# Performance work log

Measured on AMD Instinct MI355X. Metric: run time of the kernel, lower is better.

Reference implementation:

```python
import jax, jax.numpy as jnp
import numpy as np

TOP_K = 2  # module uses global top_k=2

def setup_inputs() -> dict:
    key = jax.random.key(0)
    k1, k2, k3 = jax.random.split(key, 3)
    B, S, D, E = 4, 4096, 2048, 64
    x = jax.random.normal(k1, (B, S, D), dtype=jnp.float32)
    W = jax.random.normal(k2, (E, D), dtype=jnp.float32) * 0.02  # gate_linear weight (no bias)
    noise_weight = jnp.zeros((E,), dtype=jnp.float32)  # nn.Parameter(torch.zeros(E))
    noise = jax.random.normal(k3, (B, S, E), dtype=jnp.float32)  # randn_like(logits) * noisy_std(=1.0)
    return {"x": x, "W": W, "noise_weight": noise_weight, "noise": noise}

def reference(x, W, noise_weight, noise):
    # logits = gate_linear(x)
    logits = jnp.einsum('bsd,ed->bse', x, W)
    # noisy logits: noise * noise_weight (per-expert scale), added to logits
    logits_noisy = logits + noise * noise_weight
    # top-k (largest, sorted descending, like torch.topk)
    top_vals, top_idx = jax.lax.top_k(logits_noisy, TOP_K)  # [B,S,k]
    B, S, E = logits_noisy.shape
    # scatter top-k values into -inf tensor along expert dim
    sparse = jnp.full_like(logits_noisy, -jnp.inf)
    b_ix = jnp.arange(B)[:, None, None]
    s_ix = jnp.arange(S)[None, :, None]
    sparse = sparse.at[b_ix, s_ix, top_idx].set(top_vals)
    # softmax over experts; exp(-inf)=0 zeros out non-selected experts
    gated_probs = jax.nn.softmax(sparse, axis=-1)
    return (gated_probs, top_idx, top_vals)
```

## Files before the change

kernel.cpp:

```cpp
#include <hip/hip_runtime.h>
#include <math.h>


typedef __attribute__((ext_vector_type(8))) __bf16 bf16x8;
typedef __attribute__((ext_vector_type(8))) unsigned short u16x8;
typedef __attribute__((ext_vector_type(4))) float f32x4;

constexpr int EXPN = 64;
constexpr int BM   = 32;
constexpr int BK   = 64;
constexpr int LDK  = BK + 8;

__device__ __forceinline__ void split2(float f, unsigned short& h, unsigned short& l) {
    const unsigned b = __float_as_uint(f);
    h = (unsigned short)(b >> 16);
    const float fh = __uint_as_float(b & 0xffff0000u);
    l = (unsigned short)(__float_as_uint(f - fh) >> 16);
}

__global__ __launch_bounds__(256)
void moe_gate_kernel(const float* __restrict__ x,
                     const float* __restrict__ W,
                     const float* __restrict__ nw,
                     const float* __restrict__ noise,
                     float* __restrict__ probs,
                     float* __restrict__ idx_out,
                     float* __restrict__ val_out,
                     int D)
{
    __shared__ unsigned short xh[2][BM][LDK], xl[2][BM][LDK];
    __shared__ unsigned short wh[2][EXPN][LDK], wl[2][EXPN][LDK];
    __shared__ float ls[BM][EXPN + 1];

    const int tid  = threadIdx.x;
    const int lane = tid & 63;
    const int wv   = tid >> 6;
    const int hh   = wv & 1;
    const int qq   = wv >> 1;
    const int m0   = blockIdx.x * BM;

    const int xrow = tid >> 3;
    const int xcol = (tid & 7) * 8;
    const int wrow = tid >> 2;
    const int wcol = (tid & 3) * 16;

    const float* xbase = x + (size_t)(m0 + xrow) * D + xcol;
    const float* wbase = W + (size_t)wrow * D + wcol;

    f32x4 acc0 = {0.f, 0.f, 0.f, 0.f};
    f32x4 acc1 = {0.f, 0.f, 0.f, 0.f};

    float4 xr0, xr1, wr0, wr1, wr2, wr3;
    xr0 = *(const float4*)(xbase);
    xr1 = *(const float4*)(xbase + 4);
    wr0 = *(const float4*)(wbase);
    wr1 = *(const float4*)(wbase + 4);
    wr2 = *(const float4*)(wbase + 8);
    wr3 = *(const float4*)(wbase + 12);

    const int nchunk = D / BK;
    const int fr = lane & 15;
    const int kq = (lane >> 4) * 8;

    for (int c = 0; c < nchunk; ++c) {
        const int buf = c & 1;

        {
            const float xv[8] = {xr0.x, xr0.y, xr0.z, xr0.w,
                                 xr1.x, xr1.y, xr1.z, xr1.w};
            u16x8 hv, lv;
#pragma unroll
            for (int i = 0; i < 8; ++i) {
                unsigned short a, b; split2(xv[i], a, b);
                hv[i] = a; lv[i] = b;
            }
            *(u16x8*)&xh[buf][xrow][xcol] = hv;
            *(u16x8*)&xl[buf][xrow][xcol] = lv;

            const float wvv[16] = {wr0.x, wr0.y, wr0.z, wr0.w,
                                   wr1.x, wr1.y, wr1.z, wr1.w,
                                   wr2.x, wr2.y, wr2.z, wr2.w,
                                   wr3.x, wr3.y, wr3.z, wr3.w};
            u16x8 h0, l0, h1, l1;
#pragma unroll
            for (int i = 0; i < 8; ++i) {
                unsigned short a, b; split2(wvv[i], a, b);
                h0[i] = a; l0[i] = b;
                split2(wvv[i + 8], a, b);
                h1[i] = a; l1[i] = b;
            }
            *(u16x8*)&wh[buf][wrow][wcol]     = h0;
            *(u16x8*)&wl[buf][wrow][wcol]     = l0;
            *(u16x8*)&wh[buf][wrow][wcol + 8] = h1;
            *(u16x8*)&wl[buf][wrow][wcol + 8] = l1;
        }
        __syncthreads();

        if (c + 1 < nchunk) {
            const float* xp = xbase + (c + 1) * BK;
            xr0 = *(const float4*)(xp);
            xr1 = *(const float4*)(xp + 4);
            const float* wp = wbase + (c + 1) * BK;
            wr0 = *(const float4*)(wp);
            wr1 = *(const float4*)(wp + 4);
            wr2 = *(const float4*)(wp + 8);
            wr3 = *(const float4*)(wp + 12);
        }

#pragma unroll
        for (int ks = 0; ks < BK; ks += 32) {
            const bf16x8 ah  = *(const bf16x8*)&xh[buf][hh * 16 + fr][ks + kq];
            const bf16x8 al  = *(const bf16x8*)&xl[buf][hh * 16 + fr][ks + kq];
            const bf16x8 b0h = *(const bf16x8*)&wh[buf][qq * 32 + fr][ks + kq];
            const bf16x8 b0l = *(const bf16x8*)&wl[buf][qq * 32 + fr][ks + kq];
            const bf16x8 b1h = *(const bf16x8*)&wh[buf][qq * 32 + 16 + fr][ks + kq];
            const bf16x8 b1l = *(const bf16x8*)&wl[buf][qq * 32 + 16 + fr][ks + kq];
            acc0 = __builtin_amdgcn_mfma_f32_16x16x32_bf16(ah, b0h, acc0, 0, 0, 0);
            acc0 = __builtin_amdgcn_mfma_f32_16x16x32_bf16(ah, b0l, acc0, 0, 0, 0);
            acc0 = __builtin_amdgcn_mfma_f32_16x16x32_bf16(al, b0h, acc0, 0, 0, 0);
            acc1 = __builtin_amdgcn_mfma_f32_16x16x32_bf16(ah, b1h, acc1, 0, 0, 0);
            acc1 = __builtin_amdgcn_mfma_f32_16x16x32_bf16(ah, b1l, acc1, 0, 0, 0);
            acc1 = __builtin_amdgcn_mfma_f32_16x16x32_bf16(al, b1h, acc1, 0, 0, 0);
        }
    }

    const int trow = hh * 16 + (lane >> 4) * 4;
#pragma unroll
    for (int r = 0; r < 4; ++r) {
        ls[trow + r][qq * 32 + fr]      = acc0[r];
        ls[trow + r][qq * 32 + 16 + fr] = acc1[r];
    }
    __syncthreads();

    const float nwv = nw[lane];

#pragma unroll 1
    for (int t = 0; t < 8; ++t) {
        const int tl = wv * 8 + t;
        const int g  = m0 + tl;
        const float logit = fmaf(noise[(size_t)g * EXPN + lane], nwv, ls[tl][lane]);

        float v0; int i0;
        {
            float v = logit; int ix = lane;
#pragma unroll
            for (int off = 32; off; off >>= 1) {
                const float vo = __shfl_xor(v, off);
                const int   io = __shfl_xor(ix, off);
                if (vo > v || (vo == v && io < ix)) { v = vo; ix = io; }
            }
            v0 = v; i0 = ix;
        }
        float v1; int i1;
        {
            float v = (lane == i0) ? -INFINITY : logit; int ix = lane;
#pragma unroll
            for (int off = 32; off; off >>= 1) {
                const float vo = __shfl_xor(v, off);
                const int   io = __shfl_xor(ix, off);
                if (vo > v || (vo == v && io < ix)) { v = vo; ix = io; }
            }
            v1 = v; i1 = ix;
        }
        float v2; int i2;
        {
            float v = (lane == i0 || lane == i1) ? -INFINITY : logit; int ix = lane;
#pragma unroll
            for (int off = 32; off; off >>= 1) {
                const float vo = __shfl_xor(v, off);
                const int   io = __shfl_xor(ix, off);
                if (vo > v || (vo == v && io < ix)) { v = vo; ix = io; }
            }
            v2 = v; i2 = ix;
        }

        const float eps = 1e-3f;
        if ((v0 - v1) < eps || (v1 - v2) < eps) {
            const float* xr  = x + (size_t)g * D;
            const float* w0r = W + (size_t)i0 * D;
            const float* w1r = W + (size_t)i1 * D;
            const float* w2r = W + (size_t)i2 * D;
            double s0 = 0.0, s1 = 0.0, s2 = 0.0;
            for (int d = lane; d < D; d += 64) {
                const double xv = (double)xr[d];
                s0 += xv * (double)w0r[d];
                s1 += xv * (double)w1r[d];
                s2 += xv * (double)w2r[d];
            }
#pragma unroll
            for (int off = 32; off; off >>= 1) {
                s0 += __shfl_xor(s0, off);
                s1 += __shfl_xor(s1, off);
                s2 += __shfl_xor(s2, off);
            }
            double d0 = s0 + (double)noise[(size_t)g * EXPN + i0] * (double)nw[i0];
            double d1 = s1 + (double)noise[(size_t)g * EXPN + i1] * (double)nw[i1];
            double d2 = s2 + (double)noise[(size_t)g * EXPN + i2] * (double)nw[i2];
            #define CSWAP(va, ia, vb, ib)                                   \
                if ((vb > va) || (vb == va && ib < ia)) {                   \
                    double tv = va; va = vb; vb = tv;                       \
                    int ti = ia; ia = ib; ib = ti; }
            CSWAP(d0, i0, d1, i1)
            CSWAP(d1, i1, d2, i2)
            CSWAP(d0, i0, d1, i1)
            #undef CSWAP
            v0 = (float)d0; v1 = (float)d1;
        }

        const float e1  = expf(v1 - v0);
        const float inv = 1.0f / (1.0f + e1);

        float p = 0.f;
        if (lane == i0)      p = inv;
        else if (lane == i1) p = e1 * inv;
        probs[(size_t)g * EXPN + lane] = p;

        if (lane == 0) {
            idx_out[(size_t)g * 2 + 0] = (float)i0;
            idx_out[(size_t)g * 2 + 1] = (float)i1;
            val_out[(size_t)g * 2 + 0] = v0;
            val_out[(size_t)g * 2 + 1] = v1;
        }
    }
}

extern "C" void kernel_launch(void* const* d_in, const int* in_sizes, int n_in,
                              void* d_out, int out_size, void* d_ws, size_t ws_size,
                              hipStream_t stream) {
    const float* x     = (const float*)d_in[0];
    const float* W     = (const float*)d_in[1];
    const float* nw    = (const float*)d_in[2];
    const float* noise = (const float*)d_in[3];

    const int M = in_sizes[3] / EXPN;
    const int D = in_sizes[0] / M;

    float* probs   = (float*)d_out;
    float* idx_out = probs + (size_t)M * EXPN;
    float* val_out = idx_out + (size_t)M * 2;

    const int grid = M / BM;
    moe_gate_kernel<<<grid, 256, 0, stream>>>(x, W, nw, noise,
                                              probs, idx_out, val_out, D);
}
```

Baseline: 235.5 us.

## Pre-split W into bf16 hi/lo once and deepen global prefetch to two stages

```diff
diff --git a/kernel.cpp b/kernel.cpp
--- a/kernel.cpp
+++ b/kernel.cpp
@@ -19,8 +19,26 @@
 }
 
 __global__ __launch_bounds__(256)
+void convert_w_kernel(const float* __restrict__ W,
+                      unsigned short* __restrict__ whp,
+                      unsigned short* __restrict__ wlp, int n4)
+{
+    const int i = blockIdx.x * 256 + threadIdx.x;
+    if (i >= n4) return;
+    const float4 v = *(const float4*)(W + (size_t)i * 4);
+    const float f[4] = {v.x, v.y, v.z, v.w};
+    unsigned short h[4], l[4];
+#pragma unroll
+    for (int j = 0; j < 4; ++j) split2(f[j], h[j], l[j]);
+    *(ushort4*)(whp + (size_t)i * 4) = make_ushort4(h[0], h[1], h[2], h[3]);
+    *(ushort4*)(wlp + (size_t)i * 4) = make_ushort4(l[0], l[1], l[2], l[3]);
+}
+
+__global__ __launch_bounds__(256)
 void moe_gate_kernel(const float* __restrict__ x,
                      const float* __restrict__ W,
+                     const unsigned short* __restrict__ whp,
+                     const unsigned short* __restrict__ wlp,
                      const float* __restrict__ nw,
                      const float* __restrict__ noise,
                      float* __restrict__ probs,
@@ -44,19 +62,29 @@
     const int wrow = tid >> 2;
     const int wcol = (tid & 3) * 16;
 
-    const float* xbase = x + (size_t)(m0 + xrow) * D + xcol;
-    const float* wbase = W + (size_t)wrow * D + wcol;
+    const float*          xbase  = x   + (size_t)(m0 + xrow) * D + xcol;
+    const unsigned short* whbase = whp + (size_t)wrow * D + wcol;
+    const unsigned short* wlbase = wlp + (size_t)wrow * D + wcol;
 
     f32x4 acc0 = {0.f, 0.f, 0.f, 0.f};
     f32x4 acc1 = {0.f, 0.f, 0.f, 0.f};
 
-    float4 xr0, xr1, wr0, wr1, wr2, wr3;
-    xr0 = *(const float4*)(xbase);
-    xr1 = *(const float4*)(xbase + 4);
-    wr0 = *(const float4*)(wbase);
-    wr1 = *(const float4*)(wbase + 4);
-    wr2 = *(const float4*)(wbase + 8);
-    wr3 = *(const float4*)(wbase + 12);
+    float4 px0[2], px1[2];
+    u16x8  pwh0[2], pwh1[2], pwl0[2], pwl1[2];
+
+    px0[0]  = *(const float4*)(xbase);
+    px1[0]  = *(const float4*)(xbase + 4);
+    pwh0[0] = *(const u16x8*)(whbase);
+    pwh1[0] = *(const u16x8*)(whbase + 8);
+    pwl0[0] = *(const u16x8*)(wlbase);
+    pwl1[0] = *(const u16x8*)(wlbase + 8);
+
+    px0[1]  = *(const float4*)(xbase + BK);
+    px1[1]  = *(const float4*)(xbase + BK + 4);
+    pwh0[1] = *(const u16x8*)(whbase + BK);
+    pwh1[1] = *(const u16x8*)(whbase + BK + 8);
+    pwl0[1] = *(const u16x8*)(wlbase + BK);
+    pwl1[1] = *(const u16x8*)(wlbase + BK + 8);
 
     const int nchunk = D / BK;
     const int fr = lane & 15;
@@ -66,8 +94,8 @@
         const int buf = c & 1;
 
         {
-            const float xv[8] = {xr0.x, xr0.y, xr0.z, xr0.w,
-                                 xr1.x, xr1.y, xr1.z, xr1.w};
+            const float xv[8] = {px0[buf].x, px0[buf].y, px0[buf].z, px0[buf].w,
+                                 px1[buf].x, px1[buf].y, px1[buf].z, px1[buf].w};
             u16x8 hv, lv;
 #pragma unroll
             for (int i = 0; i < 8; ++i) {
@@ -77,34 +105,21 @@
             *(u16x8*)&xh[buf][xrow][xcol] = hv;
             *(u16x8*)&xl[buf][xrow][xcol] = lv;
 
-            const float wvv[16] = {wr0.x, wr0.y, wr0.z, wr0.w,
-                                   wr1.x, wr1.y, wr1.z, wr1.w,
-                                   wr2.x, wr2.y, wr2.z, wr2.w,
-                                   wr3.x, wr3.y, wr3.z, wr3.w};
-            u16x8 h0, l0, h1, l1;
-#pragma unroll
-            for (int i = 0; i < 8; ++i) {
-                unsigned short a, b; split2(wvv[i], a, b);
-                h0[i] = a; l0[i] = b;
-                split2(wvv[i + 8], a, b);
-                h1[i] = a; l1[i] = b;
-            }
-            *(u16x8*)&wh[buf][wrow][wcol]     = h0;
-            *(u16x8*)&wl[buf][wrow][wcol]     = l0;
-            *(u16x8*)&wh[buf][wrow][wcol + 8] = h1;
-            *(u16x8*)&wl[buf][wrow][wcol + 8] = l1;
+            *(u16x8*)&wh[buf][wrow][wcol]     = pwh0[buf];
+            *(u16x8*)&wh[buf][wrow][wcol + 8] = pwh1[buf];
+            *(u16x8*)&wl[buf][wrow][wcol]     = pwl0[buf];
+            *(u16x8*)&wl[buf][wrow][wcol + 8] = pwl1[buf];
         }
         __syncthreads();
 
-        if (c + 1 < nchunk) {
-            const float* xp = xbase + (c + 1) * BK;
-            xr0 = *(const float4*)(xp);
-            xr1 = *(const float4*)(xp + 4);
-            const float* wp = wbase + (c + 1) * BK;
-            wr0 = *(const float4*)(wp);
-            wr1 = *(const float4*)(wp + 4);
-            wr2 = *(const float4*)(wp + 8);
-            wr3 = *(const float4*)(wp + 12);
+        if (c + 2 < nchunk) {
+            const int ko = (c + 2) * BK;
+            px0[buf]  = *(const float4*)(xbase + ko);
+            px1[buf]  = *(const float4*)(xbase + ko + 4);
+            pwh0[buf] = *(const u16x8*)(whbase + ko);
+            pwh1[buf] = *(const u16x8*)(whbase + ko + 8);
+            pwl0[buf] = *(const u16x8*)(wlbase + ko);
+            pwl1[buf] = *(const u16x8*)(wlbase + ko + 8);
         }
 
 #pragma unroll
@@ -234,12 +249,19 @@
 
     const int M = in_sizes[3] / EXPN;
     const int D = in_sizes[0] / M;
+    const int wn = in_sizes[1];
+
+    unsigned short* whp = (unsigned short*)d_ws;
+    unsigned short* wlp = whp + (size_t)wn;
 
     float* probs   = (float*)d_out;
     float* idx_out = probs + (size_t)M * EXPN;
     float* val_out = idx_out + (size_t)M * 2;
 
+    const int n4 = wn / 4;
+    convert_w_kernel<<<(n4 + 255) / 256, 256, 0, stream>>>(W, whp, wlp, n4);
+
     const int grid = M / BM;
-    moe_gate_kernel<<<grid, 256, 0, stream>>>(x, W, nw, noise,
+    moe_gate_kernel<<<grid, 256, 0, stream>>>(x, W, whp, wlp, nw, noise,
                                               probs, idx_out, val_out, D);
 }
```

New measurement: 377.9 us. +60.5%, slower.
